# Kernel tuning notes

Hardware: AMD Instinct MI355X
Metric: run time of the kernel (lower is better)

The kernel has to match this reference:

```python
import jax, jax.numpy as jnp
import numpy as np

CH = 512
HEADS = 8
REDUCTION = 2
INNER = max(CH // REDUCTION, HEADS)  # 256
POS_RES = 16
LN_EPS = 1e-5


def setup_inputs() -> dict:
    key = jax.random.key(0)
    ks = jax.random.split(key, 7)
    B, H, W = 1, 64, 64
    x = jax.random.normal(ks[0], (B, CH, H, W), dtype=jnp.float32)
    w_qkv = jax.random.normal(ks[1], (INNER * 3, CH), dtype=jnp.float32) * 0.02
    w_proj = jax.random.normal(ks[2], (CH, INNER), dtype=jnp.float32) * 0.02
    b_proj = jnp.zeros((CH,), dtype=jnp.float32)
    pos_bias = jax.random.normal(ks[3], (1, HEADS, POS_RES, POS_RES), dtype=jnp.float32) * 0.02
    gamma = jnp.ones((CH,), dtype=jnp.float32)
    beta = jnp.zeros((CH,), dtype=jnp.float32)
    return {"x": x, "w_qkv": w_qkv, "w_proj": w_proj, "b_proj": b_proj,
            "pos_bias": pos_bias, "gamma": gamma, "beta": beta}


def reference(x, w_qkv, w_proj, b_proj, pos_bias, gamma, beta):
    B, C, H, W = x.shape
    d_head = INNER // HEADS
    scale = jnp.float32(d_head ** -0.5)

    # 1x1 conv == channel matmul
    qkv = jnp.einsum('oc,bchw->bohw', w_qkv, x)  # [B, 3*inner, H, W]
    q, k, v = jnp.split(qkv, 3, axis=1)

    def heads_view(t):
        return t.reshape(B, HEADS, d_head, H * W)  # [B, h, d, HW]

    q, k, v = heads_view(q), heads_view(k), heads_view(v)

    attn = jnp.einsum('bhdi,bhdj->bhij', q * scale, k)  # [B, h, HW, HW]

    # bilinear interp of pos bias 16x16 -> HxW (half-pixel, matches align_corners=False)
    pos = jax.image.resize(pos_bias, (1, HEADS, H, W), method='bilinear')
    pos = pos.reshape(1, HEADS, H * W)
    attn = attn + pos[..., :, None] + pos[..., None, :]

    attn = jax.nn.softmax(attn, axis=-1)
    y = jnp.einsum('bhij,bhdj->bhdi', attn, v)  # [B, h, d, HW]
    y = y.reshape(B, INNER, H, W)

    y = jnp.einsum('co,bohw->bchw', w_proj, y) + b_proj[None, :, None, None]

    # LayerNorm over channel dim of (x + y)
    z = (x + y).transpose(0, 2, 3, 1)  # [B, H, W, C]
    mu = jnp.mean(z, axis=-1, keepdims=True)
    var = jnp.var(z, axis=-1, keepdims=True)
    z = (z - mu) / jnp.sqrt(var + LN_EPS) * gamma + beta
    return z.transpose(0, 3, 1, 2)
```

## Files before the change

kernel.cpp:

```cpp
#include <hip/hip_runtime.h>
#include <hip/hip_bf16.h>
#include <math.h>

#define HW 4096
#define LN_EPS 1e-5f

typedef _Float16 half4v __attribute__((ext_vector_type(4)));
typedef _Float16 half8v __attribute__((ext_vector_type(8)));
typedef float float4v __attribute__((ext_vector_type(4)));
typedef __fp16 fp16v2 __attribute__((ext_vector_type(2)));

#if __has_builtin(__builtin_amdgcn_exp2f)
#define EXP2F(x) __builtin_amdgcn_exp2f(x)
#else
#define EXP2F(x) exp2f(x)
#endif

__device__ __forceinline__ void gload_lds16(const _Float16* g, _Float16* l) {
#if __has_builtin(__builtin_amdgcn_global_load_lds)
    __builtin_amdgcn_global_load_lds(
        (const __attribute__((address_space(1))) void*)(const void*)g,
        (__attribute__((address_space(3))) void*)(void*)l, 16, 0, 0);
#else
    int lane = threadIdx.x & 63;
    *(half8v*)(l + lane * 8) = *(const half8v*)g;
#endif
}

__global__ __launch_bounds__(256) void k_pre(const float* __restrict__ x,
                                             const float* __restrict__ wq,
                                             const float* __restrict__ wp,
                                             const float* __restrict__ pb,
                                             _Float16* __restrict__ xt,
                                             _Float16* __restrict__ wqh,
                                             _Float16* __restrict__ wph,
                                             float* __restrict__ pos) {
    int bx = blockIdx.x, t = threadIdx.x;
    if (bx < 512) {
        __shared__ _Float16 tile[64][65];
        int c0 = (bx >> 6) * 64, p0 = (bx & 63) * 64;
        int w = t >> 6, lane = t & 63;
        #pragma unroll
        for (int r = 0; r < 16; r++)
            tile[w * 16 + r][lane] = (_Float16)x[(c0 + w * 16 + r) * HW + p0 + lane];
        __syncthreads();
        int cg = (t & 15) * 4, pr = t >> 4;
        #pragma unroll
        for (int r = 0; r < 4; r++) {
            int p = pr + r * 16;
            half4v v;
            #pragma unroll
            for (int k = 0; k < 4; k++) v[k] = tile[cg + k][p];
            *(half4v*)&xt[(p0 + p) * 512 + c0 + cg] = v;
        }
        return;
    }
    int i = (bx - 512) * 256 + t;
    const float qs = 0.17677669529663687f * 1.4426950408889634f;
    if (i < 49152) {
        float s = (i < 16384) ? qs : 1.0f;
        float4v a = *(const float4v*)(wq + i * 8);
        float4v b = *(const float4v*)(wq + i * 8 + 4);
        half8v h;
        #pragma unroll
        for (int k = 0; k < 4; k++) { h[k] = (_Float16)(a[k] * s); h[4 + k] = (_Float16)(b[k] * s); }
        *(half8v*)(wqh + i * 8) = h;
    } else if (i < 65536) {
        int j = i - 49152;
        float4v a = *(const float4v*)(wp + j * 8);
        float4v b = *(const float4v*)(wp + j * 8 + 4);
        half8v h;
        #pragma unroll
        for (int k = 0; k < 4; k++) { h[k] = (_Float16)a[k]; h[4 + k] = (_Float16)b[k]; }
        *(half8v*)(wph + j * 8) = h;
    } else {
        int j = i - 65536;
        int h = j >> 12, p = j & 4095, y = p >> 6, xx = p & 63;
        float sy = y * 0.25f - 0.375f, sx = xx * 0.25f - 0.375f;
        float fy = floorf(sy), fx = floorf(sx);
        float wy = sy - fy, wx = sx - fx;
        int y0 = (int)fy, x0 = (int)fx;
        int y1 = y0 + 1 < 15 ? y0 + 1 : 15;
        int x1 = x0 + 1 < 15 ? x0 + 1 : 15;
        y0 = y0 > 0 ? y0 : 0;
        x0 = x0 > 0 ? x0 : 0;
        const float* src = pb + h * 256;
        float v = (1.f - wy) * ((1.f - wx) * src[y0 * 16 + x0] + wx * src[y0 * 16 + x1]) +
                  wy * ((1.f - wx) * src[y1 * 16 + x0] + wx * src[y1 * 16 + x1]);
        pos[j] = v * 1.4426950408889634f;
    }
}

__global__ __launch_bounds__(256) void k_qkv(const _Float16* __restrict__ wqh,
                                             const _Float16* __restrict__ xt,
                                             _Float16* __restrict__ qa,
                                             _Float16* __restrict__ ka,
                                             _Float16* __restrict__ va) {
    int n0 = (blockIdx.x >> 5) * 64;
    int p0 = (blockIdx.x & 31) * 128;
    int t = threadIdx.x, w = t >> 6, lane = t & 63, quad = lane >> 4, l16 = lane & 15;

    const _Float16* aptr0 = xt + (p0 + w * 16 + l16) * 512 + quad * 8;
    const _Float16* aptr1 = aptr0 + 64 * 512;
    const _Float16* bptr = wqh + (n0 + l16) * 512 + quad * 8;

    float4v acc[2][4] = {};
    #pragma unroll 4
    for (int kc = 0; kc < 16; kc++) {
        half8v a0 = *(const half8v*)(aptr0 + kc * 32);
        half8v a1 = *(const half8v*)(aptr1 + kc * 32);
        #pragma unroll
        for (int nt = 0; nt < 4; nt++) {
            half8v b = *(const half8v*)(bptr + nt * 16 * 512 + kc * 32);
            acc[0][nt] = __builtin_amdgcn_mfma_f32_16x16x32_f16(a0, b, acc[0][nt], 0, 0, 0);
            acc[1][nt] = __builtin_amdgcn_mfma_f32_16x16x32_f16(a1, b, acc[1][nt], 0, 0, 0);
        }
    }
    #pragma unroll
    for (int ps = 0; ps < 2; ps++) {
        #pragma unroll
        for (int nt = 0; nt < 4; nt++) {
            int o = n0 + nt * 16 + l16;
            #pragma unroll
            for (int r = 0; r < 4; r++) {
                int p = p0 + ps * 64 + w * 16 + quad * 4 + r;
                _Float16 v = (_Float16)acc[ps][nt][r];
                if (o < 256) {
                    qa[(o >> 5) * 131072 + p * 32 + (o & 31)] = v;
                } else if (o < 512) {
                    int oc = o - 256, hh = oc >> 5, d = oc & 31;
                    int p5 = p & 31, pair = p >> 5;
                    int window = (p5 >> 2) & 1;
                    int localrow = (p5 >> 3) * 4 + (p5 & 3);
                    ka[hh * 131072 + (pair * 2 + window) * 512 +
                       ((d >> 3) * 16 + localrow) * 8 + (d & 7)] = v;
                } else {
                    int oc = o - 512, hh = oc >> 5, d = oc & 31;
                    int p5 = p & 31, pair = p >> 5;
                    va[hh * 131072 + pair * 1024 + (d >> 4) * 512 +
                       ((p5 >> 3) * 16 + (d & 15)) * 8 + (p5 & 7)] = v;
                }
            }
        }
    }
}

__global__ __launch_bounds__(256, 4) void k_attn(const _Float16* __restrict__ qa,
                                                 const _Float16* __restrict__ ka,
                                                 const _Float16* __restrict__ va,
                                                 const float* __restrict__ pos,
                                                 _Float16* __restrict__ op,
                                                 float* __restrict__ lp) {
    __shared__ __attribute__((aligned(16))) _Float16 kbuf[2][4096];
    __shared__ __attribute__((aligned(16))) _Float16 vbuf[2][4096];
    __shared__ __attribute__((aligned(16))) float posl[1024];
    int h = blockIdx.x & 7;
    int jq = (blockIdx.x >> 3) & 3;
    int qb = blockIdx.x >> 5;
    int t = threadIdx.x, w = t >> 6, lane = t & 63, quad = lane >> 4, l16 = lane & 15;
    int q0 = qb * 128 + w * 32;

    _Float16* opp = op + jq * 1048576;
    float* lpp = lp + jq * 32768;

    *(float4v*)(posl + t * 4) = *(const float4v*)(pos + h * HW + jq * 1024 + t * 4);

    half8v qf0 = *(const half8v*)(qa + h * 131072 + (q0 + l16) * 32 + quad * 8);
    half8v qf1 = *(const half8v*)(qa + h * 131072 + (q0 + 16 + l16) * 32 + quad * 8);

    const _Float16* kg = ka + h * 131072 + jq * 32768;
    const _Float16* vg = va + h * 131072 + jq * 32768;

    gload_lds16(kg + (w * 64 + lane) * 8, &kbuf[0][w * 512]);
    gload_lds16(kg + 2048 + (w * 64 + lane) * 8, &kbuf[0][2048 + w * 512]);
    gload_lds16(vg + (w * 64 + lane) * 8, &vbuf[0][w * 512]);
    gload_lds16(vg + 2048 + (w * 64 + lane) * 8, &vbuf[0][2048 + w * 512]);

    float4v o00 = {}, o01 = {}, o10 = {}, o11 = {};
    float4v lacc0 = {}, lacc1 = {};
    const half8v ones8 = {(_Float16)1.f, (_Float16)1.f, (_Float16)1.f, (_Float16)1.f,
                          (_Float16)1.f, (_Float16)1.f, (_Float16)1.f, (_Float16)1.f};

    for (int tile = 0; tile < 8; tile++) {
        int buf = tile & 1;
        __syncthreads();
        if (tile + 1 < 8) {
            const _Float16* kn = kg + (tile + 1) * 4096;
            const _Float16* vn = vg + (tile + 1) * 4096;
            gload_lds16(kn + (w * 64 + lane) * 8, &kbuf[buf ^ 1][w * 512]);
            gload_lds16(kn + 2048 + (w * 64 + lane) * 8, &kbuf[buf ^ 1][2048 + w * 512]);
            gload_lds16(vn + (w * 64 + lane) * 8, &vbuf[buf ^ 1][w * 512]);
            gload_lds16(vn + 2048 + (w * 64 + lane) * 8, &vbuf[buf ^ 1][2048 + w * 512]);
        }
        #pragma unroll
        for (int pp = 0; pp < 4; pp++) {
            const _Float16* kb = &kbuf[buf][pp * 1024];
            const _Float16* vb = &vbuf[buf][pp * 1024];
            half8v kf0 = *(const half8v*)(kb + lane * 8);
            half8v kf1 = *(const half8v*)(kb + 512 + lane * 8);
            half8v vlo = *(const half8v*)(vb + lane * 8);
            half8v vhi = *(const half8v*)(vb + 512 + lane * 8);
            float4v pb0 = *(const float4v*)(posl + tile * 128 + pp * 32 + quad * 8);
            float4v pb1 = *(const float4v*)(posl + tile * 128 + pp * 32 + quad * 8 + 4);

            __builtin_amdgcn_s_setprio(1);
            float4v s00 = __builtin_amdgcn_mfma_f32_16x16x32_f16(kf0, qf0, pb0, 0, 0, 0);
            float4v s01 = __builtin_amdgcn_mfma_f32_16x16x32_f16(kf0, qf1, pb0, 0, 0, 0);
            float4v s10 = __builtin_amdgcn_mfma_f32_16x16x32_f16(kf1, qf0, pb1, 0, 0, 0);
            float4v s11 = __builtin_amdgcn_mfma_f32_16x16x32_f16(kf1, qf1, pb1, 0, 0, 0);
            __builtin_amdgcn_s_setprio(0);

            float e0 = EXP2F(s00[0]), e1 = EXP2F(s00[1]), e2 = EXP2F(s00[2]), e3 = EXP2F(s00[3]);
            float e4 = EXP2F(s10[0]), e5 = EXP2F(s10[1]), e6 = EXP2F(s10[2]), e7 = EXP2F(s10[3]);
            float f0 = EXP2F(s01[0]), f1 = EXP2F(s01[1]), f2 = EXP2F(s01[2]), f3 = EXP2F(s01[3]);
            float f4 = EXP2F(s11[0]), f5 = EXP2F(s11[1]), f6 = EXP2F(s11[2]), f7 = EXP2F(s11[3]);

            fp16v2 a01 = __builtin_amdgcn_cvt_pkrtz(e0, e1);
            fp16v2 a23 = __builtin_amdgcn_cvt_pkrtz(e2, e3);
            fp16v2 a45 = __builtin_amdgcn_cvt_pkrtz(e4, e5);
            fp16v2 a67 = __builtin_amdgcn_cvt_pkrtz(e6, e7);
            fp16v2 b01 = __builtin_amdgcn_cvt_pkrtz(f0, f1);
            fp16v2 b23 = __builtin_amdgcn_cvt_pkrtz(f2, f3);
            fp16v2 b45 = __builtin_amdgcn_cvt_pkrtz(f4, f5);
            fp16v2 b67 = __builtin_amdgcn_cvt_pkrtz(f6, f7);

            half4v pA0 = __builtin_bit_cast(half4v, __builtin_shufflevector(a01, a23, 0, 1, 2, 3));
            half4v pA1 = __builtin_bit_cast(half4v, __builtin_shufflevector(a45, a67, 0, 1, 2, 3));
            half8v pa0 = __builtin_shufflevector(pA0, pA1, 0, 1, 2, 3, 4, 5, 6, 7);
            half4v pB0 = __builtin_bit_cast(half4v, __builtin_shufflevector(b01, b23, 0, 1, 2, 3));
            half4v pB1 = __builtin_bit_cast(half4v, __builtin_shufflevector(b45, b67, 0, 1, 2, 3));
            half8v pa1 = __builtin_shufflevector(pB0, pB1, 0, 1, 2, 3, 4, 5, 6, 7);

            __builtin_amdgcn_s_setprio(1);
            o00 = __builtin_amdgcn_mfma_f32_16x16x32_f16(pa0, vlo, o00, 0, 0, 0);
            o01 = __builtin_amdgcn_mfma_f32_16x16x32_f16(pa0, vhi, o01, 0, 0, 0);
            o10 = __builtin_amdgcn_mfma_f32_16x16x32_f16(pa1, vlo, o10, 0, 0, 0);
            o11 = __builtin_amdgcn_mfma_f32_16x16x32_f16(pa1, vhi, o11, 0, 0, 0);
            lacc0 = __builtin_amdgcn_mfma_f32_16x16x32_f16(pa0, ones8, lacc0, 0, 0, 0);
            lacc1 = __builtin_amdgcn_mfma_f32_16x16x32_f16(pa1, ones8, lacc1, 0, 0, 0);
            __builtin_amdgcn_s_setprio(0);
        }
    }
    #pragma unroll
    for (int r = 0; r < 4; r++) {
        int qr = quad * 4 + r;
        int qi0 = q0 + qr, qi1 = q0 + 16 + qr;
        opp[qi0 * 256 + h * 32 + l16] = (_Float16)o00[r];
        opp[qi0 * 256 + h * 32 + 16 + l16] = (_Float16)o01[r];
        opp[qi1 * 256 + h * 32 + l16] = (_Float16)o10[r];
        opp[qi1 * 256 + h * 32 + 16 + l16] = (_Float16)o11[r];
    }
    if (l16 == 0) {
        #pragma unroll
        for (int r = 0; r < 4; r++) {
            lpp[(q0 + quad * 4 + r) * 8 + h] = lacc0[r];
            lpp[(q0 + 16 + quad * 4 + r) * 8 + h] = lacc1[r];
        }
    }
}

__global__ __launch_bounds__(1024) void k_proj_ln(const _Float16* __restrict__ wph,
                                                  const _Float16* __restrict__ op,
                                                  const float* __restrict__ lp,
                                                  const float* __restrict__ x,
                                                  const float* __restrict__ b_proj,
                                                  const float* __restrict__ gamma,
                                                  const float* __restrict__ beta,
                                                  float* __restrict__ out) {
    __shared__ __attribute__((aligned(16))) _Float16 ys[16 * 264];
    __shared__ float red[2][16][17];
    int p0 = blockIdx.x * 16;
    int t = threadIdx.x, w = t >> 6, lane = t & 63, quad = lane >> 4, l16 = lane & 15;
    {
        int p = t >> 6, cg = (t & 63) * 4;
        int pi = p0 + p;
        half4v a0 = *(const half4v*)(op + pi * 256 + cg);
        half4v a1 = *(const half4v*)(op + 1048576 + pi * 256 + cg);
        half4v a2 = *(const half4v*)(op + 2097152 + pi * 256 + cg);
        half4v a3 = *(const half4v*)(op + 3145728 + pi * 256 + cg);
        int hh = cg >> 5;
        float l = lp[pi * 8 + hh] + lp[32768 + pi * 8 + hh] +
                  lp[65536 + pi * 8 + hh] + lp[98304 + pi * 8 + hh];
        float inv = 1.f / l;
        half4v y;
        #pragma unroll
        for (int k = 0; k < 4; k++)
            y[k] = (_Float16)((((float)a0[k] + (float)a1[k]) +
                               ((float)a2[k] + (float)a3[k])) * inv);
        *(half4v*)(ys + p * 264 + cg) = y;
    }
    __syncthreads();
    float4v acc[2] = {};
    #pragma unroll
    for (int kc = 0; kc < 8; kc++) {
        half8v b = *(const half8v*)(ys + l16 * 264 + kc * 32 + quad * 8);
        #pragma unroll
        for (int mt = 0; mt < 2; mt++) {
            half8v a = *(const half8v*)(wph + (w * 32 + mt * 16 + l16) * 256 + kc * 32 + quad * 8);
            acc[mt] = __builtin_amdgcn_mfma_f32_16x16x32_f16(a, b, acc[mt], 0, 0, 0);
        }
    }
    int p = p0 + l16;
    float sum = 0.f, sumsq = 0.f;
    #pragma unroll
    for (int mt = 0; mt < 2; mt++)
        #pragma unroll
        for (int r = 0; r < 4; r++) {
            int c = w * 32 + mt * 16 + quad * 4 + r;
            float v = acc[mt][r] + b_proj[c] + x[c * HW + p];
            acc[mt][r] = v;
            sum += v;
            sumsq += v * v;
        }
    sum += __shfl_xor(sum, 16, 64);
    sum += __shfl_xor(sum, 32, 64);
    sumsq += __shfl_xor(sumsq, 16, 64);
    sumsq += __shfl_xor(sumsq, 32, 64);
    if (quad == 0) { red[0][w][l16] = sum; red[1][w][l16] = sumsq; }
    __syncthreads();
    float s0 = 0.f, s1 = 0.f;
    #pragma unroll
    for (int ww = 0; ww < 16; ww++) { s0 += red[0][ww][l16]; s1 += red[1][ww][l16]; }
    float mean = s0 * (1.f / 512.f);
    float var = s1 * (1.f / 512.f) - mean * mean;
    float rstd = rsqrtf(var + LN_EPS);
    #pragma unroll
    for (int mt = 0; mt < 2; mt++)
        #pragma unroll
        for (int r = 0; r < 4; r++) {
            int c = w * 32 + mt * 16 + quad * 4 + r;
            out[c * HW + p] = (acc[mt][r] - mean) * rstd * gamma[c] + beta[c];
        }
}

extern "C" void kernel_launch(void* const* d_in, const int* in_sizes, int n_in,
                              void* d_out, int out_size, void* d_ws, size_t ws_size,
                              hipStream_t stream) {
    const float* x      = (const float*)d_in[0];
    const float* w_qkv  = (const float*)d_in[1];
    const float* w_proj = (const float*)d_in[2];
    const float* b_proj = (const float*)d_in[3];
    const float* pos_b  = (const float*)d_in[4];
    const float* gamma  = (const float*)d_in[5];
    const float* beta   = (const float*)d_in[6];
    char* ws = (char*)d_ws;
    _Float16* xt  = (_Float16*)(ws);
    _Float16* qa  = (_Float16*)(ws + 4194304);
    _Float16* ka  = (_Float16*)(ws + 6291456);
    _Float16* va  = (_Float16*)(ws + 8388608);
    _Float16* op  = (_Float16*)(ws + 10485760);
    float*    lp  = (float*)   (ws + 18874368);
    float*    pos = (float*)   (ws + 19398656);
    _Float16* wqh = (_Float16*)(ws + 19529728);
    _Float16* wph = (_Float16*)(ws + 20316160);

    k_pre<<<896, 256, 0, stream>>>(x, w_qkv, w_proj, pos_b, xt, wqh, wph, pos);
    k_qkv<<<384, 256, 0, stream>>>(wqh, xt, qa, ka, va);
    k_attn<<<1024, 256, 0, stream>>>(qa, ka, va, pos, op, lp);
    k_proj_ln<<<256, 1024, 0, stream>>>(wph, op, lp, x, b_proj, gamma, beta, (float*)d_out);
}
```

Before: 133.9 us.

## Load K/V and position bias directly from global memory in attention kernel

Removes the LDS double-buffered staging of K/V tiles and the LDS copy of the position bias. Each wave now reads its MFMA fragments straight from global memory, relying on L1/L2 caching, and the loop is unrolled by two. The intent is to drop the per-tile __syncthreads and LDS traffic and free LDS for occupancy. The cost is that four waves in a block re-fetch the same K/V data through cache, and without explicit prefetch, global-load latency may be exposed.

Result: no change. 136.5 us (+2.0%).

```diff
diff --git a/kernel.cpp b/kernel.cpp
--- a/kernel.cpp
+++ b/kernel.cpp
@@ -15,17 +15,6 @@
 #else
 #define EXP2F(x) exp2f(x)
 #endif
-
-__device__ __forceinline__ void gload_lds16(const _Float16* g, _Float16* l) {
-#if __has_builtin(__builtin_amdgcn_global_load_lds)
-    __builtin_amdgcn_global_load_lds(
-        (const __attribute__((address_space(1))) void*)(const void*)g,
-        (__attribute__((address_space(3))) void*)(void*)l, 16, 0, 0);
-#else
-    int lane = threadIdx.x & 63;
-    *(half8v*)(l + lane * 8) = *(const half8v*)g;
-#endif
-}
 
 __global__ __launch_bounds__(256) void k_pre(const float* __restrict__ x,
                                              const float* __restrict__ wq,
@@ -151,9 +140,6 @@
                                                  const float* __restrict__ pos,
                                                  _Float16* __restrict__ op,
                                                  float* __restrict__ lp) {
-    __shared__ __attribute__((aligned(16))) _Float16 kbuf[2][4096];
-    __shared__ __attribute__((aligned(16))) _Float16 vbuf[2][4096];
-    __shared__ __attribute__((aligned(16))) float posl[1024];
     int h = blockIdx.x & 7;
     int jq = (blockIdx.x >> 3) & 3;
     int qb = blockIdx.x >> 5;
@@ -163,45 +149,30 @@
     _Float16* opp = op + jq * 1048576;
     float* lpp = lp + jq * 32768;
 
-    *(float4v*)(posl + t * 4) = *(const float4v*)(pos + h * HW + jq * 1024 + t * 4);
-
     half8v qf0 = *(const half8v*)(qa + h * 131072 + (q0 + l16) * 32 + quad * 8);
     half8v qf1 = *(const half8v*)(qa + h * 131072 + (q0 + 16 + l16) * 32 + quad * 8);
 
     const _Float16* kg = ka + h * 131072 + jq * 32768;
     const _Float16* vg = va + h * 131072 + jq * 32768;
-
-    gload_lds16(kg + (w * 64 + lane) * 8, &kbuf[0][w * 512]);
-    gload_lds16(kg + 2048 + (w * 64 + lane) * 8, &kbuf[0][2048 + w * 512]);
-    gload_lds16(vg + (w * 64 + lane) * 8, &vbuf[0][w * 512]);
-    gload_lds16(vg + 2048 + (w * 64 + lane) * 8, &vbuf[0][2048 + w * 512]);
+    const float* pq = pos + h * HW + jq * 1024;
 
     float4v o00 = {}, o01 = {}, o10 = {}, o11 = {};
     float4v lacc0 = {}, lacc1 = {};
     const half8v ones8 = {(_Float16)1.f, (_Float16)1.f, (_Float16)1.f, (_Float16)1.f,
                           (_Float16)1.f, (_Float16)1.f, (_Float16)1.f, (_Float16)1.f};
 
+    #pragma unroll 2
     for (int tile = 0; tile < 8; tile++) {
-        int buf = tile & 1;
-        __syncthreads();
-        if (tile + 1 < 8) {
-            const _Float16* kn = kg + (tile + 1) * 4096;
-            const _Float16* vn = vg + (tile + 1) * 4096;
-            gload_lds16(kn + (w * 64 + lane) * 8, &kbuf[buf ^ 1][w * 512]);
-            gload_lds16(kn + 2048 + (w * 64 + lane) * 8, &kbuf[buf ^ 1][2048 + w * 512]);
-            gload_lds16(vn + (w * 64 + lane) * 8, &vbuf[buf ^ 1][w * 512]);
-            gload_lds16(vn + 2048 + (w * 64 + lane) * 8, &vbuf[buf ^ 1][2048 + w * 512]);
-        }
         #pragma unroll
         for (int pp = 0; pp < 4; pp++) {
-            const _Float16* kb = &kbuf[buf][pp * 1024];
-            const _Float16* vb = &vbuf[buf][pp * 1024];
+            const _Float16* kb = kg + tile * 4096 + pp * 1024;
+            const _Float16* vb = vg + tile * 4096 + pp * 1024;
             half8v kf0 = *(const half8v*)(kb + lane * 8);
             half8v kf1 = *(const half8v*)(kb + 512 + lane * 8);
             half8v vlo = *(const half8v*)(vb + lane * 8);
             half8v vhi = *(const half8v*)(vb + 512 + lane * 8);
-            float4v pb0 = *(const float4v*)(posl + tile * 128 + pp * 32 + quad * 8);
-            float4v pb1 = *(const float4v*)(posl + tile * 128 + pp * 32 + quad * 8 + 4);
+            float4v pb0 = *(const float4v*)(pq + tile * 128 + pp * 32 + quad * 8);
+            float4v pb1 = *(const float4v*)(pq + tile * 128 + pp * 32 + quad * 8 + 4);
 
             __builtin_amdgcn_s_setprio(1);
             float4v s00 = __builtin_amdgcn_mfma_f32_16x16x32_f16(kf0, qf0, pb0, 0, 0, 0);
```
